# Optimization experiments

Measured on AMD Instinct MI355X. Metric: run time of the kernel, lower is better.

Reference implementation:

```python
import jax, jax.numpy as jnp
import numpy as np

B, T, D_MODEL, N_HEADS = 2, 2048, 1024, 16
HEAD_DIM = D_MODEL // N_HEADS
GN_EPS = 1e-5


def decay_gammas(n_heads):
    # gamma_h = 1 - 2^(-5 - h*(8/n_heads))
    h = jnp.arange(n_heads, dtype=jnp.float32)
    return 1.0 - jnp.power(2.0, -5.0 - h * (8.0 / n_heads))


def setup_inputs() -> dict:
    key = jax.random.key(0)
    ks = jax.random.split(key, 7)
    w_scale = 0.02
    return {
        "x": jax.random.normal(ks[0], (B, T, D_MODEL), dtype=jnp.float32),
        "Wq": jax.random.normal(ks[1], (D_MODEL, D_MODEL), dtype=jnp.float32) * w_scale,
        "Wk": jax.random.normal(ks[2], (D_MODEL, D_MODEL), dtype=jnp.float32) * w_scale,
        "Wv": jax.random.normal(ks[3], (D_MODEL, D_MODEL), dtype=jnp.float32) * w_scale,
        "Wo": jax.random.normal(ks[4], (D_MODEL, D_MODEL), dtype=jnp.float32) * w_scale,
        "gn_w": jnp.ones((D_MODEL,), dtype=jnp.float32),
        "gn_b": jnp.zeros((D_MODEL,), dtype=jnp.float32),
    }


def reference(x, Wq, Wk, Wv, Wo, gn_w, gn_b):
    Bx, Tx, C = x.shape
    H, D = N_HEADS, C // N_HEADS
    gammas = decay_gammas(H)  # (H,)

    def split_heads(y):
        return y.reshape(Bx, Tx, H, D).transpose(0, 2, 1, 3)  # (B,H,T,D)

    # torch Linear: y = x @ W.T
    Q = split_heads(x @ Wq.T)
    K = split_heads(x @ Wk.T)
    V = split_heads(x @ Wv.T)

    # causal decay mask D[h,i,j] = gamma_h^(i-j) if i>=j else 0
    idx = jnp.arange(Tx, dtype=jnp.float32)
    diff = idx[:, None] - idx[None, :]  # (T,T)
    mask = jnp.where(diff >= 0,
                     gammas[:, None, None] ** jnp.maximum(diff, 0.0),
                     0.0)  # (H,T,T)

    scores = jnp.einsum("bhtd,bhsd->bhts", Q, K) / jnp.sqrt(jnp.float32(D))
    scores = scores * mask[None]  # (B,H,T,T)
    out = jnp.einsum("bhts,bhsd->bhtd", scores, V)  # (B,H,T,D)
    y = out.transpose(0, 2, 1, 3).reshape(Bx, Tx, C)  # merge heads

    # GroupNorm(n_heads, d_model) applied on (B, C, T): normalizes over
    # (head_dim, T) per group per batch element.
    z = y.transpose(0, 2, 1).reshape(Bx, H, D, Tx)
    mu = z.mean(axis=(2, 3), keepdims=True)
    var = z.var(axis=(2, 3), keepdims=True)
    zn = (z - mu) * jax.lax.rsqrt(var + GN_EPS)
    zn = zn * gn_w.reshape(1, H, D, 1) + gn_b.reshape(1, H, D, 1)
    y = zn.reshape(Bx, C, Tx).transpose(0, 2, 1)  # (B,T,C)

    return y @ Wo.T
```

## Files before the change

kernel.cpp:

```cpp
#include <hip/hip_runtime.h>
#include <hip/hip_bf16.h>

typedef __attribute__((ext_vector_type(8))) short short8;
typedef __attribute__((ext_vector_type(4))) float float4v;
typedef __attribute__((ext_vector_type(16))) float float16v;
typedef unsigned short u16;
typedef unsigned long long ull;

#define KD 1024

__device__ __forceinline__ u16 f2b(float f) {
    __hip_bfloat16 h = __float2bfloat16(f);
    return __builtin_bit_cast(u16, h);
}
__device__ __forceinline__ float b2f(u16 u) {
    unsigned x = ((unsigned)u) << 16;
    return __builtin_bit_cast(float, x);
}
__device__ __forceinline__ float lg_gamma(int h) {
    float gamma = 1.0f - exp2f(-5.0f - 0.5f * (float)h);
    return log2f(gamma);
}

__device__ __forceinline__ void async_cp16(const u16* g, u16* l) {
    __builtin_amdgcn_global_load_lds(
        (const __attribute__((address_space(1))) void*)g,
        (__attribute__((address_space(3))) void*)l,
        16, 0, 0);
}

__global__ __launch_bounds__(256)
void cvt_all(const float* __restrict__ x, const float* __restrict__ wq,
             const float* __restrict__ wk, const float* __restrict__ wv,
             const float* __restrict__ wo,
             u16* __restrict__ xb, u16* __restrict__ wqkvb, u16* __restrict__ wob)
{
    int bid = blockIdx.x;
    if (bid < 4096) {
        long i = (long)bid * 1024 + threadIdx.x * 4;
        float4 v = *(const float4*)(x + i);
        ushort4 u;
        u.x = f2b(v.x); u.y = f2b(v.y); u.z = f2b(v.z); u.w = f2b(v.w);
        *(ushort4*)(xb + i) = u;
    } else {
        int wbid = bid - 4096;
        int mtx = wbid >> 8;
        int panel = (wbid & 255) >> 3, ks = wbid & 7;
        const float* src = (mtx == 0) ? wq : (mtx == 1) ? wk : (mtx == 2) ? wv : wo;
        u16* dst = (mtx == 3) ? wob : (wqkvb + (size_t)mtx * 1048576);
        float sc = (mtx == 0) ? 0.125f : 1.0f;
        int idx = threadIdx.x * 16;
        int kg = idx >> 9, kh = (idx >> 8) & 1, r0 = (idx & 255) >> 3;
        int k0 = ks * 128 + kg * 16 + kh * 8;
        int row = panel * 32 + r0;
        const float* s0 = src + (size_t)row * 1024 + k0;
        float4 a0 = ((const float4*)s0)[0], a1 = ((const float4*)s0)[1];
        float4 b0 = ((const float4*)(s0 + 1024))[0], b1 = ((const float4*)(s0 + 1024))[1];
        short8 o0, o1;
        o0[0]=f2b(a0.x*sc); o0[1]=f2b(a0.y*sc); o0[2]=f2b(a0.z*sc); o0[3]=f2b(a0.w*sc);
        o0[4]=f2b(a1.x*sc); o0[5]=f2b(a1.y*sc); o0[6]=f2b(a1.z*sc); o0[7]=f2b(a1.w*sc);
        o1[0]=f2b(b0.x*sc); o1[1]=f2b(b0.y*sc); o1[2]=f2b(b0.z*sc); o1[3]=f2b(b0.w*sc);
        o1[4]=f2b(b1.x*sc); o1[5]=f2b(b1.y*sc); o1[6]=f2b(b1.z*sc); o1[7]=f2b(b1.w*sc);
        u16* d = dst + (size_t)panel * 32768 + ks * 4096 + idx;
        *(short8*)d = o0;
        *(short8*)(d + 8) = o1;
    }
}

template<int MODE>
__global__ __launch_bounds__(256)
void gemm_nt(const u16* __restrict__ A, const u16* __restrict__ Bpk,
             u16* __restrict__ oQ, u16* __restrict__ oK,
             u16* __restrict__ oKt, u16* __restrict__ oVt,
             float* __restrict__ of)
{
    constexpr int TM = (MODE == 0) ? 128 : 64;
    constexpr int MI = (MODE == 0) ? 2 : 1;
    __shared__ __attribute__((aligned(16))) u16 Sh[(MODE == 0) ? 16384 : 4096];
    u16* As = Sh;
    const int tid = threadIdx.x;
    const int lane = tid & 63;
    const int wv = tid >> 6;
    const int wm = wv >> 1, wn = wv & 1;
    const int row32 = lane & 31, khalf = lane >> 5;
    const int lrow = lane >> 3, lseg = lane & 7;
    const int lin = blockIdx.x;
    const int xcd = lin & 7, idx = lin >> 3;
    int m_tile, n_tile;
    if (MODE == 0) { m_tile = idx & 31; n_tile = xcd * 3 + (idx >> 5); }
    else           { m_tile = idx;      n_tile = xcd; }
    const int m0 = m_tile * TM, n0 = n_tile * 128;

    float16v acc[MI][2];
#pragma unroll
    for (int i = 0; i < MI; i++)
#pragma unroll
        for (int j = 0; j < 2; j++)
#pragma unroll
            for (int r = 0; r < 16; r++) acc[i][j][r] = 0.f;

    const int scol = (lseg ^ lrow) << 3;
    const u16* bp = Bpk + (size_t)((n0 >> 5) + wn * 2) * 32768 + (size_t)lane * 8;

    for (int kt = 0; kt < KD; kt += 64) {
        __syncthreads();
#pragma unroll
        for (int i = 0; i < TM / 32; i++) {
            int r = wv * (TM / 4) + i * 8;
            async_cp16(A + (size_t)(m0 + r + lrow) * KD + kt + scol, &As[r * 64]);
        }
        short8 bgl[4][2];
#pragma unroll
        for (int ks = 0; ks < 4; ks++)
#pragma unroll
            for (int j = 0; j < 2; j++)
                bgl[ks][j] = *(const short8*)(bp + (size_t)j * 32768 + ((kt >> 4) + ks) * 512);
        __syncthreads();
#pragma unroll
        for (int ks = 0; ks < 4; ks++) {
            short8 af[MI];
#pragma unroll
            for (int i = 0; i < MI; i++) {
                int row = wm * (MI * 32) + i * 32 + row32;
                af[i] = *(const short8*)(&As[row * 64 + (((ks * 2 + khalf) ^ (row & 7)) << 3)]);
            }
#pragma unroll
            for (int i = 0; i < MI; i++)
#pragma unroll
                for (int j = 0; j < 2; j++)
                    acc[i][j] = __builtin_amdgcn_mfma_f32_32x32x16_bf16(af[i], bgl[ks][j], acc[i][j], 0, 0, 0);
        }
    }

    if (MODE == 0) {
        const int wsel = n0 >> 10;
        if (wsel <= 1) {
            u16* dst = (wsel == 0) ? oQ : oK;
#pragma unroll
            for (int i = 0; i < 2; i++)
#pragma unroll
                for (int j = 0; j < 2; j++) {
                    int gn = n0 + wn * 64 + j * 32 + row32;
                    int dd = gn & 63, hh = (gn >> 6) & 15;
#pragma unroll
                    for (int reg = 0; reg < 16; reg++) {
                        int m = m0 + wm * 64 + i * 32 + (reg & 3) + 8 * (reg >> 2) + 4 * khalf;
                        int b = m >> 11, t = m & 2047;
                        dst[(size_t)(b * 16 + hh) * 131072 + t * 64 + dd] = f2b(acc[i][j][reg]);
                    }
                }
        }
        if (wsel >= 1) {
            __syncthreads();
            u16* Tl = Sh + wv * 4096;
#pragma unroll
            for (int i = 0; i < 2; i++)
#pragma unroll
                for (int j = 0; j < 2; j++) {
                    int n_loc = j * 32 + row32;
#pragma unroll
                    for (int g = 0; g < 4; g++) {
                        int m4 = i * 32 + 8 * g + 4 * khalf;
                        ull pk = (ull)f2b(acc[i][j][4 * g]) | ((ull)f2b(acc[i][j][4 * g + 1]) << 16) |
                                 ((ull)f2b(acc[i][j][4 * g + 2]) << 32) | ((ull)f2b(acc[i][j][4 * g + 3]) << 48);
                        *(ull*)(&Tl[n_loc * 64 + (((m4 >> 3) ^ (n_loc & 7)) << 3) + (m4 & 7)]) = pk;
                    }
                }
            __syncthreads();
            int gnb = n0 + wn * 64;
            int hh = (gnb >> 6) & 15;
            int mb = m0 + wm * 64;
            int bh = (mb >> 11) * 16 + hh;
            int t0 = mb & 2047;
            u16* dstT = (wsel == 1) ? oKt : oVt;
            int rr = lane >> 3, ss = lane & 7;
#pragma unroll
            for (int g = 0; g < 8; g++) {
                int row = 8 * g + rr;
                short8 v = *(const short8*)(&Tl[row * 64 + ((ss ^ rr) << 3)]);
                *(short8*)(&dstT[(size_t)bh * 131072 + (size_t)row * 2048 + t0 + ss * 8]) = v;
            }
        }
    } else {
        int gn0 = n0 + wn * 64 + row32;
#pragma unroll
        for (int g = 0; g < 4; g++)
#pragma unroll
            for (int rr = 0; rr < 4; rr++) {
                int reg = 4 * g + rr;
                int m = m0 + wm * 32 + 8 * g + 4 * khalf + rr;
                of[(size_t)m * 1024 + gn0] = acc[0][0][reg];
                of[(size_t)m * 1024 + gn0 + 32] = acc[0][1][reg];
            }
    }
}

__global__ __launch_bounds__(256)
void chunk_state(const u16* __restrict__ Kt, const u16* __restrict__ Vt,
                 u16* __restrict__ U)
{
    const int c = blockIdx.x, bh = blockIdx.y, h = bh & 15;
    const int tid = threadIdx.x, lane = tid & 63, w = tid >> 6;
    const int row16 = lane & 15, quad = lane >> 4;
    const float lg = lg_gamma(h);
    const size_t base = (size_t)bh * 131072;

    float4v acc[4];
    float4v zero4 = {0.f, 0.f, 0.f, 0.f};
#pragma unroll
    for (int tn = 0; tn < 4; tn++) acc[tn] = zero4;

#pragma unroll
    for (int kb = 0; kb < 2; kb++) {
        short8 a = *(const short8*)(Vt + base + (size_t)(16 * w + row16) * 2048 + c * 64 + kb * 32 + quad * 8);
        short8 as;
        int e0 = 63 - (kb * 32 + quad * 8);
#pragma unroll
        for (int jj = 0; jj < 8; jj++) {
            float v = b2f((u16)a[jj]) * exp2f(lg * (float)(e0 - jj));
            as[jj] = (short)f2b(v);
        }
#pragma unroll
        for (int tn = 0; tn < 4; tn++) {
            short8 bfr = *(const short8*)(Kt + base + (size_t)(16 * tn + row16) * 2048 + c * 64 + kb * 32 + quad * 8);
            acc[tn] = __builtin_amdgcn_mfma_f32_16x16x32_bf16(as, bfr, acc[tn], 0, 0, 0);
        }
    }
    u16* up = U + ((size_t)bh * 32 + c) * 4096;
#pragma unroll
    for (int tn = 0; tn < 4; tn++)
#pragma unroll
        for (int r = 0; r < 4; r++)
            up[(16 * w + quad * 4 + r) * 64 + 16 * tn + row16] = f2b(acc[tn][r]);
}

__global__ __launch_bounds__(256)
void state_scan(const u16* __restrict__ U, u16* __restrict__ St)
{
    const int bh = blockIdx.y;
    const int e = blockIdx.x * 256 + threadIdx.x;
    const float g64 = exp2f(lg_gamma(bh & 15) * 64.0f);
    float s = 0.f;
    St[(size_t)bh * 131072 + e] = 0;
    for (int c = 1; c < 32; c++) {
        s = g64 * s + b2f(U[((size_t)bh * 32 + (c - 1)) * 4096 + e]);
        St[((size_t)bh * 32 + c) * 4096 + e] = f2b(s);
    }
}

__global__ __launch_bounds__(256)
void retention_chunk(const u16* __restrict__ Q, const u16* __restrict__ Kb,
                     const u16* __restrict__ Vt, const u16* __restrict__ St,
                     u16* __restrict__ Y, float* __restrict__ stats)
{
    __shared__ __attribute__((aligned(16))) u16 Pl[4][16 * 72];
    __shared__ float red[8];
    const int c = blockIdx.x, bh = blockIdx.y, h = bh & 15;
    const int tid = threadIdx.x, lane = tid & 63, w = tid >> 6;
    const int row16 = lane & 15, quad = lane >> 4;
    const float lg = lg_gamma(h);
    const size_t base = (size_t)bh * 131072;
    float4v zero4 = {0.f, 0.f, 0.f, 0.f};

    short8 qf[2];
#pragma unroll
    for (int kb = 0; kb < 2; kb++)
        qf[kb] = *(const short8*)(Q + base + (size_t)(c * 64 + 16 * w + row16) * 64 + kb * 32 + quad * 8);

    float4v accp[4];
#pragma unroll
    for (int tn = 0; tn < 4; tn++) accp[tn] = zero4;
#pragma unroll
    for (int tn = 0; tn < 4; tn++)
#pragma unroll
        for (int kb = 0; kb < 2; kb++) {
            short8 kf = *(const short8*)(Kb + base + (size_t)(c * 64 + 16 * tn + row16) * 64 + kb * 32 + quad * 8);
            accp[tn] = __builtin_amdgcn_mfma_f32_16x16x32_bf16(qf[kb], kf, accp[tn], 0, 0, 0);
        }
#pragma unroll
    for (int tn = 0; tn < 4; tn++)
#pragma unroll
        for (int r = 0; r < 4; r++) {
            int a_loc = 16 * w + quad * 4 + r;
            int b_loc = 16 * tn + row16;
            int d = a_loc - b_loc;
            float v = (d >= 0) ? accp[tn][r] * exp2f(lg * (float)d) : 0.f;
            Pl[w][(quad * 4 + r) * 72 + b_loc] = f2b(v);
        }
    __syncthreads();

    short8 pf[2];
#pragma unroll
    for (int kb = 0; kb < 2; kb++)
        pf[kb] = *(const short8*)(&Pl[w][row16 * 72 + kb * 32 + quad * 8]);

    float4v acco[4], acci[4];
#pragma unroll
    for (int tn = 0; tn < 4; tn++) { acco[tn] = zero4; acci[tn] = zero4; }
#pragma unroll
    for (int tn = 0; tn < 4; tn++)
#pragma unroll
        for (int kb = 0; kb < 2; kb++) {
            short8 vf = *(const short8*)(Vt + base + (size_t)(16 * tn + row16) * 2048 + c * 64 + kb * 32 + quad * 8);
            acco[tn] = __builtin_amdgcn_mfma_f32_16x16x32_bf16(pf[kb], vf, acco[tn], 0, 0, 0);
            short8 sf = *(const short8*)(St + ((size_t)bh * 32 + c) * 4096 + (16 * tn + row16) * 64 + kb * 32 + quad * 8);
            acci[tn] = __builtin_amdgcn_mfma_f32_16x16x32_bf16(qf[kb], sf, acci[tn], 0, 0, 0);
        }

    float s = 0.f, s2 = 0.f;
#pragma unroll
    for (int tn = 0; tn < 4; tn++)
#pragma unroll
        for (int r = 0; r < 4; r++) {
            int a_loc = 16 * w + quad * 4 + r;
            float gi = exp2f(lg * (float)(a_loc + 1));
            int t = c * 64 + a_loc, d2 = 16 * tn + row16;
            float yv = acco[tn][r] + gi * acci[tn][r];
            Y[(size_t)bh * 131072 + t * 64 + d2] = f2b(yv);
            s += yv;
            s2 += yv * yv;
        }
#pragma unroll
    for (int off = 32; off; off >>= 1) {
        s += __shfl_down(s, off, 64);
        s2 += __shfl_down(s2, off, 64);
    }
    if (lane == 0) { red[w] = s; red[4 + w] = s2; }
    __syncthreads();
    if (tid == 0) {
        atomicAdd(&stats[2 * bh], red[0] + red[1] + red[2] + red[3]);
        atomicAdd(&stats[2 * bh + 1], red[4] + red[5] + red[6] + red[7]);
    }
}

__global__ __launch_bounds__(256)
void gn_apply(const u16* __restrict__ Y, const float* __restrict__ stats,
              const float* __restrict__ gnw, const float* __restrict__ gnb,
              u16* __restrict__ Z)
{
    int i4 = (blockIdx.x * 256 + threadIdx.x) * 4;
    int b = i4 >> 21, t = (i4 >> 10) & 2047, cc = i4 & 1023;
    int hh = cc >> 6, dd = cc & 63, bh = b * 16 + hh;
    ushort4 yv4 = *(const ushort4*)(Y + (size_t)bh * 131072 + t * 64 + dd);
    float S = stats[2 * bh], S2 = stats[2 * bh + 1];
    float mu = S * (1.0f / 131072.f);
    float var = S2 * (1.0f / 131072.f) - mu * mu;
    float rsg = rsqrtf(var + 1e-5f);
    float4 wv = *(const float4*)(gnw + cc);
    float4 bv = *(const float4*)(gnb + cc);
    ushort4 o;
    o.x = f2b((b2f(yv4.x) - mu) * rsg * wv.x + bv.x);
    o.y = f2b((b2f(yv4.y) - mu) * rsg * wv.y + bv.y);
    o.z = f2b((b2f(yv4.z) - mu) * rsg * wv.z + bv.z);
    o.w = f2b((b2f(yv4.w) - mu) * rsg * wv.w + bv.w);
    *(ushort4*)(Z + i4) = o;
}

extern "C" void kernel_launch(void* const* d_in, const int* in_sizes, int n_in,
                              void* d_out, int out_size, void* d_ws, size_t ws_size,
                              hipStream_t stream) {
    const float* x   = (const float*)d_in[0];
    const float* Wq  = (const float*)d_in[1];
    const float* Wk  = (const float*)d_in[2];
    const float* Wv  = (const float*)d_in[3];
    const float* Wo  = (const float*)d_in[4];
    const float* gnw = (const float*)d_in[5];
    const float* gnb = (const float*)d_in[6];
    float* out = (float*)d_out;
    char* ws = (char*)d_ws;

    u16*  xb    = (u16*)(ws + 0);
    u16*  wqkvb = (u16*)(ws + 8388608);
    u16*  wob   = (u16*)(ws + 14680064);
    u16*  Qs    = (u16*)(ws + 16777216);
    u16*  Kb    = (u16*)(ws + 25165824);
    u16*  Kt    = (u16*)(ws + 33554432);
    u16*  Vt    = (u16*)(ws + 41943040);
    u16*  U     = (u16*)(ws + 50331648);
    u16*  St    = (u16*)(ws + 67108864);
    u16*  Y     = (u16*)(ws + 75497472);
    u16*  Zb    = (u16*)(ws + 92274688);
    float* stats= (float*)(ws + 100663296);

    hipMemsetAsync(stats, 0, 64 * sizeof(float), stream);

    cvt_all<<<5120, 256, 0, stream>>>(x, Wq, Wk, Wv, Wo, xb, wqkvb, wob);

    gemm_nt<0><<<768, 256, 0, stream>>>(xb, wqkvb, Qs, Kb, Kt, Vt, nullptr);

    chunk_state<<<dim3(32, 32), 256, 0, stream>>>(Kt, Vt, U);
    state_scan<<<dim3(16, 32), 256, 0, stream>>>(U, St);
    retention_chunk<<<dim3(32, 32), 256, 0, stream>>>(Qs, Kb, Vt, St, Y, stats);

    gn_apply<<<4096, 256, 0, stream>>>(Y, stats, gnw, gnb, Zb);

    gemm_nt<1><<<512, 256, 0, stream>>>(Zb, wob, nullptr, nullptr, nullptr, nullptr, out);
}
```

Measured before the change: 185.6 us.

## Fuse chunk state computation and scan into one sequential per-head kernel

Replaces the chunk_state and state_scan kernels with a single kernel in which one block per (batch, head) walks the 32 chunks in order. It computes each chunk's K^T V contribution with MFMA and accumulates the decayed state in fp32 registers. This drops the U intermediate buffer round trip and one kernel launch, but shrinks parallelism from 1024 blocks to 32 and serializes the chunks, leaving most CUs idle. It also remaps the QKV GEMM tile order so each XCD group shares M tiles instead of N tiles.

```diff
diff --git a/kernel.cpp b/kernel.cpp
--- a/kernel.cpp
+++ b/kernel.cpp
@@ -87,7 +87,7 @@
     const int lin = blockIdx.x;
     const int xcd = lin & 7, idx = lin >> 3;
     int m_tile, n_tile;
-    if (MODE == 0) { m_tile = idx & 31; n_tile = xcd * 3 + (idx >> 5); }
+    if (MODE == 0) { m_tile = (idx & 3) + 4 * xcd; n_tile = idx >> 2; }
     else           { m_tile = idx;      n_tile = xcd; }
     const int m0 = m_tile * TM, n0 = n_tile * 128;
 
@@ -196,55 +196,55 @@
 }
 
 __global__ __launch_bounds__(256)
-void chunk_state(const u16* __restrict__ Kt, const u16* __restrict__ Vt,
-                 u16* __restrict__ U)
-{
-    const int c = blockIdx.x, bh = blockIdx.y, h = bh & 15;
+void state_fused(const u16* __restrict__ Kt, const u16* __restrict__ Vt,
+                 u16* __restrict__ St)
+{
+    const int bh = blockIdx.x, h = bh & 15;
     const int tid = threadIdx.x, lane = tid & 63, w = tid >> 6;
     const int row16 = lane & 15, quad = lane >> 4;
     const float lg = lg_gamma(h);
+    const float g64 = exp2f(lg * 64.0f);
     const size_t base = (size_t)bh * 131072;
-
-    float4v acc[4];
     float4v zero4 = {0.f, 0.f, 0.f, 0.f};
-#pragma unroll
-    for (int tn = 0; tn < 4; tn++) acc[tn] = zero4;
-
-#pragma unroll
-    for (int kb = 0; kb < 2; kb++) {
-        short8 a = *(const short8*)(Vt + base + (size_t)(16 * w + row16) * 2048 + c * 64 + kb * 32 + quad * 8);
-        short8 as;
-        int e0 = 63 - (kb * 32 + quad * 8);
-#pragma unroll
-        for (int jj = 0; jj < 8; jj++) {
-            float v = b2f((u16)a[jj]) * exp2f(lg * (float)(e0 - jj));
-            as[jj] = (short)f2b(v);
-        }
-#pragma unroll
-        for (int tn = 0; tn < 4; tn++) {
-            short8 bfr = *(const short8*)(Kt + base + (size_t)(16 * tn + row16) * 2048 + c * 64 + kb * 32 + quad * 8);
-            acc[tn] = __builtin_amdgcn_mfma_f32_16x16x32_bf16(as, bfr, acc[tn], 0, 0, 0);
-        }
-    }
-    u16* up = U + ((size_t)bh * 32 + c) * 4096;
-#pragma unroll
-    for (int tn = 0; tn < 4; tn++)
-#pragma unroll
-        for (int r = 0; r < 4; r++)
-            up[(16 * w + quad * 4 + r) * 64 + 16 * tn + row16] = f2b(acc[tn][r]);
-}
-
-__global__ __launch_bounds__(256)
-void state_scan(const u16* __restrict__ U, u16* __restrict__ St)
-{
-    const int bh = blockIdx.y;
-    const int e = blockIdx.x * 256 + threadIdx.x;
-    const float g64 = exp2f(lg_gamma(bh & 15) * 64.0f);
-    float s = 0.f;
-    St[(size_t)bh * 131072 + e] = 0;
-    for (int c = 1; c < 32; c++) {
-        s = g64 * s + b2f(U[((size_t)bh * 32 + (c - 1)) * 4096 + e]);
-        St[((size_t)bh * 32 + c) * 4096 + e] = f2b(s);
+
+    float st[4][4];
+#pragma unroll
+    for (int tn = 0; tn < 4; tn++)
+#pragma unroll
+        for (int r = 0; r < 4; r++) st[tn][r] = 0.f;
+
+    for (int c = 0; c < 32; c++) {
+        u16* sc = St + ((size_t)bh * 32 + c) * 4096;
+#pragma unroll
+        for (int tn = 0; tn < 4; tn++)
+#pragma unroll
+            for (int r = 0; r < 4; r++)
+                sc[(16 * w + quad * 4 + r) * 64 + 16 * tn + row16] = f2b(st[tn][r]);
+
+        float4v acc[4];
+#pragma unroll
+        for (int tn = 0; tn < 4; tn++) acc[tn] = zero4;
+#pragma unroll
+        for (int kb = 0; kb < 2; kb++) {
+            short8 a = *(const short8*)(Vt + base + (size_t)(16 * w + row16) * 2048 + c * 64 + kb * 32 + quad * 8);
+            short8 as;
+            int e0 = 63 - (kb * 32 + quad * 8);
+#pragma unroll
+            for (int jj = 0; jj < 8; jj++) {
+                float v = b2f((u16)a[jj]) * exp2f(lg * (float)(e0 - jj));
+                as[jj] = (short)f2b(v);
+            }
+#pragma unroll
+            for (int tn = 0; tn < 4; tn++) {
+                short8 bfr = *(const short8*)(Kt + base + (size_t)(16 * tn + row16) * 2048 + c * 64 + kb * 32 + quad * 8);
+                acc[tn] = __builtin_amdgcn_mfma_f32_16x16x32_bf16(as, bfr, acc[tn], 0, 0, 0);
+            }
+        }
+#pragma unroll
+        for (int tn = 0; tn < 4; tn++)
+#pragma unroll
+            for (int r = 0; r < 4; r++)
+                st[tn][r] = g64 * st[tn][r] + acc[tn][r];
     }
 }
 
@@ -376,7 +376,6 @@
     u16*  Kb    = (u16*)(ws + 25165824);
     u16*  Kt    = (u16*)(ws + 33554432);
     u16*  Vt    = (u16*)(ws + 41943040);
-    u16*  U     = (u16*)(ws + 50331648);
     u16*  St    = (u16*)(ws + 67108864);
     u16*  Y     = (u16*)(ws + 75497472);
     u16*  Zb    = (u16*)(ws + 92274688);
@@ -388,8 +387,7 @@
 
     gemm_nt<0><<<768, 256, 0, stream>>>(xb, wqkvb, Qs, Kb, Kt, Vt, nullptr);
 
-    chunk_state<<<dim3(32, 32), 256, 0, stream>>>(Kt, Vt, U);
-    state_scan<<<dim3(16, 32), 256, 0, stream>>>(U, St);
+    state_fused<<<32, 256, 0, stream>>>(Kt, Vt, St);
     retention_chunk<<<dim3(32, 32), 256, 0, stream>>>(Qs, Kb, Vt, St, Y, stats);
 
     gn_apply<<<4096, 256, 0, stream>>>(Y, stats, gnw, gnb, Zb);
```

Result: slower. 214.9 us (+15.8%).
